# Performance work log

Hardware: AMD Instinct MI355X
Metric: run time of the kernel (lower is better)

The kernel has to match this reference:

```python
import jax, jax.numpy as jnp
import numpy as np
import math

EMBED_DIM = 512
NUM_HEADS = 8
NUM_EXPERTS = 16
TOP_K = 8
B, T = 2, 1024


def setup_inputs() -> dict:
    key = jax.random.key(0)
    ks = jax.random.split(key, 16)
    d, E = EMBED_DIM, NUM_EXPERTS
    hdim = 4 * d  # expert hidden width
    s = 0.02
    inp = {
        "x": jax.random.normal(ks[0], (B, T, d), jnp.float32),
        # RMSNorm params (init ones, matching torch module)
        "g": jnp.ones((d,), jnp.float32),
        "b": jnp.ones((d,), jnp.float32),
        # attention
        "c_attn_w": jax.random.normal(ks[1], (d, 3 * d), jnp.float32) * s,
        "c_attn_b": jnp.zeros((3 * d,), jnp.float32),
        "alpha": jnp.ones((NUM_HEADS,), jnp.float32),
        "c_proj_w": jax.random.normal(ks[2], (d, d), jnp.float32) * s,
        "c_proj_b": jnp.zeros((d,), jnp.float32),
        # router
        "router_w": jax.random.normal(ks[3], (d, E), jnp.float32) * s,
        "router_b": jnp.zeros((E,), jnp.float32),
        # stacked expert params: Linear(d,4d) -> SwiGLU(4d,4d) -> Linear(4d,d)
        "w_in": jax.random.normal(ks[4], (E, d, hdim), jnp.float32) * s,
        "b_in": jnp.zeros((E, hdim), jnp.float32),
        "w1": jax.random.normal(ks[5], (E, hdim, 2 * hdim), jnp.float32) * s,
        "b1": jnp.zeros((E, 2 * hdim), jnp.float32),
        "w2": jax.random.normal(ks[6], (E, hdim, hdim), jnp.float32) * s,
        "b2": jnp.zeros((E, hdim), jnp.float32),
        "w_out": jax.random.normal(ks[7], (E, hdim, d), jnp.float32) * s,
        "b_out": jnp.zeros((E, d), jnp.float32),
    }
    return inp


def _block(x, g, b, c_attn_w, c_attn_b, alpha, c_proj_w, c_proj_b,
           router_w, router_b, w_in, b_in, w1, b1, w2, b2, w_out, b_out):
    Bb, Tt, C = x.shape
    H = alpha.shape[0]
    hd = C // H
    E = router_b.shape[0]

    # RMSNorm (note: additive b, per original module)
    rms = jnp.sqrt(jnp.mean(x * x, axis=-1, keepdims=True) + 1e-6)
    xn = (x / rms) * g + b

    # QK-normalized causal attention
    qkv = xn @ c_attn_w + c_attn_b                      # [B,T,3C]
    q, k, v = jnp.split(qkv, 3, axis=-1)
    def heads(t):
        return t.reshape(Bb, Tt, H, hd).transpose(0, 2, 1, 3)  # [B,H,T,hd]
    q, k, v = heads(q), heads(k), heads(v)
    eps = 1e-5
    q_hat = q / (jnp.linalg.norm(q, axis=-1, keepdims=True) + eps)
    k_hat = k / (jnp.linalg.norm(k, axis=-1, keepdims=True) + eps)
    factor = (alpha * math.sqrt(hd)).reshape(1, H, 1, 1)
    q_scaled = q_hat * factor
    # SDPA default scale = 1/sqrt(head_dim)
    scores = jnp.einsum("bhqd,bhkd->bhqk", q_scaled, k_hat) / math.sqrt(hd)
    causal = jnp.tril(jnp.ones((Tt, Tt), bool))
    scores = jnp.where(causal, scores, -jnp.inf)
    att = jax.nn.softmax(scores, axis=-1)
    y = jnp.einsum("bhqk,bhkd->bhqd", att, v)
    y = y.transpose(0, 2, 1, 3).reshape(Bb, Tt, C)
    y = y @ c_proj_w + c_proj_b
    x = x + y

    # Router + top-8 normalized gates
    routes = jax.nn.softmax(x @ router_w + router_b, axis=-1)  # [B,T,E]
    probs, idx = jax.lax.top_k(routes, TOP_K)
    probs = probs / jnp.sum(probs, axis=-1, keepdims=True)
    # combine weights per expert: [B,T,E]
    gates = jnp.sum(jax.nn.one_hot(idx, E, dtype=x.dtype) * probs[..., None], axis=2)

    # Dense expert evaluation (faithful math: unselected tokens get zero gate)
    N = Bb * Tt
    xf = x.reshape(N, C)
    gf = gates.reshape(N, E)
    h = jnp.einsum("nd,edf->enf", xf, w_in) + b_in[:, None, :]      # [E,N,4d]
    c = jnp.einsum("enf,efg->eng", h, w1) + b1[:, None, :]          # [E,N,8d]
    a, bb2 = jnp.split(c, 2, axis=-1)
    s = (bb2 * jax.nn.sigmoid(bb2)) * a                              # SwiGLU
    o = jnp.einsum("enf,efg->eng", s, w2) + b2[:, None, :]          # [E,N,4d]
    eo = jnp.einsum("enf,efd->end", o, w_out) + b_out[:, None, :]   # [E,N,d]
    moe = jnp.einsum("end,ne->nd", eo, gf).reshape(Bb, Tt, C)
    return x + moe


def reference(x, g, b, c_attn_w, c_attn_b, alpha, c_proj_w, c_proj_b,
              router_w, router_b, w_in, b_in, w1, b1, w2, b2, w_out, b_out):
    return _block(x, g, b, c_attn_w, c_attn_b, alpha, c_proj_w, c_proj_b,
                  router_w, router_b, w_in, b_in, w1, b1, w2, b2, w_out, b_out)
```

## Files before the change

### kernel.cpp

```cpp
#include <hip/hip_runtime.h>
#include <stdint.h>

#define DEVI __device__ __forceinline__
#define FENCE() asm volatile("" ::: "memory")

typedef short short8 __attribute__((ext_vector_type(8)));
typedef short short4v __attribute__((ext_vector_type(4)));
typedef float f32x4 __attribute__((ext_vector_type(4)));

DEVI float bf2f(unsigned short s){ union{unsigned u; float f;} x; x.u = ((unsigned)s)<<16; return x.f; }
DEVI unsigned short f2bf(float f){ union{float f; unsigned u;} x; x.f=f; unsigned r = x.u + 0x7fff + ((x.u>>16)&1); return (unsigned short)(r>>16); }

DEVI void gload_lds16(const void* g, void* l){
  __builtin_amdgcn_global_load_lds((const __attribute__((address_space(1))) unsigned int*)g,
                                   (__attribute__((address_space(3))) unsigned int*)l, 16, 0, 0);
}

__global__ __launch_bounds__(256)
void transpose_cvt(const float* __restrict__ in, unsigned short* __restrict__ out, int K, int N)
{
  __shared__ float tile[32][33];
  size_t zoff = (size_t)blockIdx.z * K * N;
  const float* src = in + zoff;
  unsigned short* dst = out + zoff;
  int kb = blockIdx.y*32, nb = blockIdx.x*32;
  int t = threadIdx.x;
  int tr = t>>3, tc = (t&7)*4;
  float4 v = *(const float4*)(src + (size_t)(kb+tr)*N + nb + tc);
  tile[tr][tc+0]=v.x; tile[tr][tc+1]=v.y; tile[tr][tc+2]=v.z; tile[tr][tc+3]=v.w;
  __syncthreads();
  short4v ov;
  ov[0] = (short)f2bf(tile[tc+0][tr]);
  ov[1] = (short)f2bf(tile[tc+1][tr]);
  ov[2] = (short)f2bf(tile[tc+2][tr]);
  ov[3] = (short)f2bf(tile[tc+3][tr]);
  *(short4v*)(dst + (size_t)(nb+tr)*K + kb + tc) = ov;
}

__global__ __launch_bounds__(256)
void rmsnorm_k(const float* __restrict__ x, const float* __restrict__ gw,
               const float* __restrict__ bw, unsigned short* __restrict__ xn)
{
  int row = blockIdx.x*4 + (threadIdx.x>>6);
  int lane = threadIdx.x & 63;
  const float* xr = x + (size_t)row*512 + lane*8;
  float4 a = *(const float4*)xr;
  float4 c = *(const float4*)(xr+4);
  float ss = a.x*a.x+a.y*a.y+a.z*a.z+a.w*a.w + c.x*c.x+c.y*c.y+c.z*c.z+c.w*c.w;
  #pragma unroll
  for (int m=1;m<64;m<<=1) ss += __shfl_xor(ss, m);
  float inv = 1.0f / sqrtf(ss*(1.f/512.f) + 1e-6f);
  const float* gr = gw + lane*8; const float* br = bw + lane*8;
  float4 g0=*(const float4*)gr, g1=*(const float4*)(gr+4);
  float4 b0=*(const float4*)br, b1=*(const float4*)(br+4);
  short8 o;
  o[0]=(short)f2bf(a.x*inv*g0.x + b0.x);
  o[1]=(short)f2bf(a.y*inv*g0.y + b0.y);
  o[2]=(short)f2bf(a.z*inv*g0.z + b0.z);
  o[3]=(short)f2bf(a.w*inv*g0.w + b0.w);
  o[4]=(short)f2bf(c.x*inv*g1.x + b1.x);
  o[5]=(short)f2bf(c.y*inv*g1.y + b1.y);
  o[6]=(short)f2bf(c.z*inv*g1.z + b1.z);
  o[7]=(short)f2bf(c.w*inv*g1.w + b1.w);
  *(short8*)(xn + (size_t)row*512 + lane*8) = o;
}

template<int EPI>
__global__ __launch_bounds__(512, 2)
void gemm3(const unsigned short* __restrict__ A, const unsigned short* __restrict__ B,
           const float* __restrict__ bias,
           float* __restrict__ Cf, unsigned short* __restrict__ Ch,
           const unsigned short* __restrict__ aux,
           int M, int N, int K,
           const int* __restrict__ off, long long strideBz, long long strideBiasz)
{
  __shared__ char smem[147456];
  int z = blockIdx.z;
  int rowbase = 0, Mz = M;
  if (off){ rowbase = off[z]; Mz = off[z+1] - rowbase; }
  int row0 = blockIdx.y * 256;
  if (row0 >= Mz) return;
  int col0 = blockIdx.x * 128;
  const unsigned short* Ab = A + (size_t)(rowbase + row0) * K;
  const unsigned short* Bb = B + (size_t)z * strideBz + (size_t)col0 * K;
  const float* biasz = bias + (size_t)z * strideBiasz;

  int tid = threadIdx.x;
  int lane = tid & 63, w = tid >> 6;
  int lrow = lane & 15, lg = lane >> 4;
  int wr = w >> 1, wc = w & 1;

  f32x4 acc[4][4];
  #pragma unroll
  for (int i=0;i<4;i++){
    #pragma unroll
    for (int j=0;j<4;j++) acc[i][j] = f32x4{0.f,0.f,0.f,0.f};
  }

  int nkt = K >> 6;

  auto stage = [&](int kt2, int part){
    if (kt2 >= nkt) return;
    char* sA = smem + (kt2 % 3) * 49152;
    char* sB = sA + 32768;
    int k0 = kt2 << 6;
    #pragma unroll
    for (int i=0;i<2;i++){
      int s = (part*2 + i)*512 + tid;
      int r = s >> 3, kb = (s & 7) ^ (r & 7);
      gload_lds16(Ab + (size_t)r*K + k0 + kb*8, sA + s*16);
    }
    {
      int s = part*512 + tid;
      int r = s >> 3, kb = (s & 7) ^ (r & 7);
      gload_lds16(Bb + (size_t)r*K + k0 + kb*8, sB + s*16);
    }
  };

  stage(0,0); stage(0,1); stage(1,0); stage(1,1);
  asm volatile("s_waitcnt vmcnt(6)" ::: "memory");
  __builtin_amdgcn_s_barrier();
  FENCE();

  for (int kt = 0; kt < nkt; kt++){
    char* sA = smem + (kt % 3) * 49152;
    char* sB = sA + 32768;
    short8 bfr[4][2], afr[4][2];
    #pragma unroll
    for (int n=0;n<4;n++){
      int ct = wc*64 + n*16 + lrow;
      #pragma unroll
      for (int kk=0;kk<2;kk++){
        int kbb = lg + kk*4;
        bfr[n][kk] = *(const short8*)(sB + ct*128 + ((kbb ^ (ct&7))<<4));
      }
    }
    #pragma unroll
    for (int m=0;m<2;m++){
      int rt = wr*64 + m*16 + lrow;
      #pragma unroll
      for (int kk=0;kk<2;kk++){
        int kbb = lg + kk*4;
        afr[m][kk] = *(const short8*)(sA + rt*128 + ((kbb ^ (rt&7))<<4));
      }
    }
    stage(kt+2, 0);
    FENCE(); __builtin_amdgcn_s_barrier(); FENCE();
    __builtin_amdgcn_s_setprio(1);
    #pragma unroll
    for (int m=0;m<2;m++){
      #pragma unroll
      for (int n=0;n<4;n++){
        #pragma unroll
        for (int kk=0;kk<2;kk++)
          acc[m][n] = __builtin_amdgcn_mfma_f32_16x16x32_bf16(afr[m][kk], bfr[n][kk], acc[m][n], 0,0,0);
      }
    }
    __builtin_amdgcn_s_setprio(0);
    FENCE(); __builtin_amdgcn_s_barrier(); FENCE();
    #pragma unroll
    for (int m=2;m<4;m++){
      int rt = wr*64 + m*16 + lrow;
      #pragma unroll
      for (int kk=0;kk<2;kk++){
        int kbb = lg + kk*4;
        afr[m][kk] = *(const short8*)(sA + rt*128 + ((kbb ^ (rt&7))<<4));
      }
    }
    stage(kt+2, 1);
    FENCE(); __builtin_amdgcn_s_barrier(); FENCE();
    __builtin_amdgcn_s_setprio(1);
    #pragma unroll
    for (int m=2;m<4;m++){
      #pragma unroll
      for (int n=0;n<4;n++){
        #pragma unroll
        for (int kk=0;kk<2;kk++)
          acc[m][n] = __builtin_amdgcn_mfma_f32_16x16x32_bf16(afr[m][kk], bfr[n][kk], acc[m][n], 0,0,0);
      }
    }
    __builtin_amdgcn_s_setprio(0);
    asm volatile("s_waitcnt vmcnt(6)" ::: "memory");
    FENCE(); __builtin_amdgcn_s_barrier(); FENCE();
  }

  #pragma unroll
  for (int m=0;m<4;m++){
    int rloc = wr*64 + m*16 + lg*4;
    #pragma unroll
    for (int j=0;j<4;j++){
      int row = row0 + rloc + j;
      if (row < Mz){
        size_t rg = (size_t)(rowbase + row);
        #pragma unroll
        for (int n=0;n<4;n++){
          int col = col0 + wc*64 + n*16 + lrow;
          float v = acc[m][n][j] + biasz[col];
          size_t idx = rg * N + col;
          if constexpr (EPI == 0){
            Cf[idx] = v;
          } else if constexpr (EPI == 1){
            Ch[idx] = f2bf(v);
          } else {
            float a = bf2f(aux[idx]);
            float sg = v / (1.f + __expf(-v));
            Ch[idx] = f2bf(a * sg);
          }
        }
      }
    }
  }
}

__global__ __launch_bounds__(256)
void gemm_proj(const unsigned short* __restrict__ A, const unsigned short* __restrict__ B,
               const float* __restrict__ bias,
               float* __restrict__ Cf, unsigned short* __restrict__ Ch,
               const float* __restrict__ resid, int M, int N, int K)
{
  __shared__ char smem[32768];
  char* smA = smem; char* smB = smem + 16384;
  int row0 = blockIdx.y * 128;
  int col0 = blockIdx.x * 128;
  int t = threadIdx.x, w = t>>6, lane = t&63;
  int lrow = lane&15, lg = lane>>4;
  int wr = w>>1, wc = w&1;

  f32x4 acc[4][4];
  #pragma unroll
  for (int i=0;i<4;i++){
    #pragma unroll
    for (int j=0;j<4;j++) acc[i][j] = f32x4{0.f,0.f,0.f,0.f};
  }
  const size_t Abase = (size_t)row0 * K;
  const size_t Bbase = (size_t)col0 * K;
  int nkt = K >> 6;
  for (int kt=0; kt<nkt; kt++){
    __syncthreads();
    int k0 = kt*64;
    #pragma unroll
    for (int i=0;i<4;i++){
      int s = (i*4 + w)*64 + lane;
      int r = s>>3;
      int kb = (s&7) ^ (r&7);
      gload_lds16(A + Abase + (size_t)r*K + k0 + kb*8, smA + (size_t)(i*4+w)*1024);
      gload_lds16(B + Bbase + (size_t)r*K + k0 + kb*8, smB + (size_t)(i*4+w)*1024);
    }
    __syncthreads();
    #pragma unroll
    for (int ks=0; ks<2; ks++){
      short8 af[4], bf[4];
      int kbb = lg + ks*4;
      #pragma unroll
      for (int m=0;m<4;m++){
        int rt = wr*64 + m*16 + lrow;
        af[m] = *(const short8*)(smA + rt*128 + ((kbb ^ (rt&7))<<4));
      }
      #pragma unroll
      for (int n=0;n<4;n++){
        int rt = wc*64 + n*16 + lrow;
        bf[n] = *(const short8*)(smB + rt*128 + ((kbb ^ (rt&7))<<4));
      }
      #pragma unroll
      for (int m=0;m<4;m++){
        #pragma unroll
        for (int n=0;n<4;n++)
          acc[m][n] = __builtin_amdgcn_mfma_f32_16x16x32_bf16(af[m], bf[n], acc[m][n], 0,0,0);
      }
    }
  }
  #pragma unroll
  for (int m=0;m<4;m++){
    int rloc = wr*64 + m*16 + lg*4;
    #pragma unroll
    for (int j=0;j<4;j++){
      int row = row0 + rloc + j;
      size_t rg = (size_t)row;
      #pragma unroll
      for (int n=0;n<4;n++){
        int col = col0 + wc*64 + n*16 + lrow;
        float v = acc[m][n][j] + bias[col];
        size_t idx = rg * N + col;
        v += resid[idx];
        Cf[idx] = v;
        Ch[idx] = f2bf(v);
      }
    }
  }
}

__global__ __launch_bounds__(256)
void prep_qkv(const float* __restrict__ qkv, const float* __restrict__ alpha,
              unsigned short* __restrict__ q_s, unsigned short* __restrict__ k_hat,
              unsigned short* __restrict__ v_t)
{
  int idx = blockIdx.x*4 + (threadIdx.x>>6);
  int lane = threadIdx.x & 63;
  int h = idx & 7, bt = idx >> 3;
  size_t base = (size_t)bt*1536 + h*64 + lane;
  float qv = qkv[base], kv = qkv[base+512], vv = qkv[base+1024];
  float qs2 = qv*qv, ks2 = kv*kv;
  #pragma unroll
  for (int m=1;m<64;m<<=1){ qs2 += __shfl_xor(qs2, m); ks2 += __shfl_xor(ks2, m); }
  float qh = qv / (sqrtf(qs2) + 1e-5f) * alpha[h];
  float kh = kv / (sqrtf(ks2) + 1e-5f);
  int b = bt >> 10, tt = bt & 1023;
  size_t hb = ((size_t)(b*8+h))*1024*64;
  q_s[hb + (size_t)tt*64 + lane] = f2bf(qh);
  k_hat[hb + (size_t)tt*64 + lane] = f2bf(kh);
  v_t[((size_t)(b*8+h)*64 + lane)*1024 + tt] = f2bf(vv);
}

__global__ __launch_bounds__(256)
void attn_k(const unsigned short* __restrict__ q_s, const unsigned short* __restrict__ k_hat,
            const unsigned short* __restrict__ v_t, unsigned short* __restrict__ y)
{
  __shared__ char sm[51200];
  char* smK = sm + 18432;
  char* smV = sm + 34816;
  int qt = blockIdx.x, bh = blockIdx.y;
  int b = bh>>3, h = bh&7;
  int t = threadIdx.x, w = t>>6, lane = t&63;
  int lrow = lane&15, lg = lane>>4;
  int q0 = qt*128;
  const size_t hQK = (size_t)bh*1024*64;
  const size_t hV  = (size_t)bh*64*1024;

  #pragma unroll
  for (int i=0;i<4;i++){
    int s = (i*4+w)*64 + lane;
    int r = s>>3, kb = (s&7)^(r&7);
    gload_lds16(q_s + hQK + (size_t)(q0+r)*64 + kb*8, sm + (size_t)(i*4+w)*1024);
  }
  __syncthreads();
  short8 qf[2][2];
  #pragma unroll
  for (int mf=0;mf<2;mf++){
    #pragma unroll
    for (int ks=0;ks<2;ks++){
      int rt = w*32 + mf*16 + lrow;
      int kbb = lg + ks*4;
      qf[mf][ks] = *(const short8*)(sm + rt*128 + ((kbb^(rt&7))<<4));
    }
  }
  f32x4 oacc[2][4];
  #pragma unroll
  for (int i=0;i<2;i++){
    #pragma unroll
    for (int j=0;j<4;j++) oacc[i][j] = f32x4{0.f,0.f,0.f,0.f};
  }
  float mrun[2][4], lrun[2][4];
  #pragma unroll
  for (int i=0;i<2;i++){
    #pragma unroll
    for (int j=0;j<4;j++){ mrun[i][j] = -1e30f; lrun[i][j] = 0.f; }
  }
  char* Pw = sm + w*4608;

  for (int kt=0; kt<=qt; kt++){
    __syncthreads();
    int t0 = kt*128;
    #pragma unroll
    for (int i=0;i<4;i++){
      int s = (i*4+w)*64 + lane;
      int r = s>>3, kb = (s&7)^(r&7);
      gload_lds16(k_hat + hQK + (size_t)(t0+r)*64 + kb*8, smK + (size_t)(i*4+w)*1024);
    }
    #pragma unroll
    for (int i=0;i<4;i++){
      int s = (i*4+w)*64 + lane;
      int d = s>>4, kb2 = s&15;
      int kb = kb2 ^ (d&7);
      gload_lds16(v_t + hV + (size_t)d*1024 + t0 + kb*8, smV + (size_t)(i*4+w)*1024);
    }
    __syncthreads();

    f32x4 sacc[2][8];
    #pragma unroll
    for (int i=0;i<2;i++){
      #pragma unroll
      for (int j=0;j<8;j++) sacc[i][j] = f32x4{0.f,0.f,0.f,0.f};
    }
    #pragma unroll
    for (int ks=0;ks<2;ks++){
      short8 kf[8];
      int kbb = lg + ks*4;
      #pragma unroll
      for (int nf=0;nf<8;nf++){
        int rt = nf*16+lrow;
        kf[nf] = *(const short8*)(smK + rt*128 + ((kbb^(rt&7))<<4));
      }
      #pragma unroll
      for (int mf=0;mf<2;mf++){
        #pragma unroll
        for (int nf=0;nf<8;nf++)
          sacc[mf][nf] = __builtin_amdgcn_mfma_f32_16x16x32_bf16(qf[mf][ks], kf[nf], sacc[mf][nf], 0,0,0);
      }
    }
    if (kt == qt){
      #pragma unroll
      for (int mf=0;mf<2;mf++){
        #pragma unroll
        for (int nf=0;nf<8;nf++){
          #pragma unroll
          for (int j=0;j<4;j++){
            int qi = w*32+mf*16+lg*4+j;
            int ki = nf*16 + lrow;
            if (ki > qi) sacc[mf][nf][j] = -1e30f;
          }
        }
      }
    }
    #pragma unroll
    for (int mf=0;mf<2;mf++){
      #pragma unroll
      for (int j=0;j<4;j++){
        float mx = sacc[mf][0][j];
        #pragma unroll
        for (int nf=1;nf<8;nf++) mx = fmaxf(mx, sacc[mf][nf][j]);
        #pragma unroll
        for (int m=1;m<16;m<<=1) mx = fmaxf(mx, __shfl_xor(mx, m));
        float mnew = fmaxf(mrun[mf][j], mx);
        float sc = __expf(mrun[mf][j] - mnew);
        float rs = 0.f;
        #pragma unroll
        for (int nf=0;nf<8;nf++){
          float p = __expf(sacc[mf][nf][j] - mnew);
          sacc[mf][nf][j] = p; rs += p;
        }
        #pragma unroll
        for (int m=1;m<16;m<<=1) rs += __shfl_xor(rs, m);
        lrun[mf][j] = lrun[mf][j]*sc + rs;
        mrun[mf][j] = mnew;
        #pragma unroll
        for (int n2=0;n2<4;n2++) oacc[mf][n2][j] *= sc;
      }
    }
    #pragma unroll
    for (int half=0; half<2; half++){
      #pragma unroll
      for (int mf=0;mf<2;mf++){
        #pragma unroll
        for (int nfh=0;nfh<4;nfh++){
          int nf = half*4 + nfh;
          #pragma unroll
          for (int j=0;j<4;j++){
            int row = mf*16 + lg*4 + j;
            int col = nfh*16 + lrow;
            *(unsigned short*)(Pw + (row*72 + col)*2) = f2bf(sacc[mf][nf][j]);
          }
        }
      }
      #pragma unroll
      for (int k2=0;k2<2;k2++){
        int ks2 = half*2 + k2;
        short8 pf[2], vf[4];
        #pragma unroll
        for (int mf=0;mf<2;mf++)
          pf[mf] = *(const short8*)(Pw + (mf*16+lrow)*144 + lg*16 + k2*64);
        #pragma unroll
        for (int n2=0;n2<4;n2++){
          int d = n2*16+lrow;
          int kbb2 = lg + ks2*4;
          vf[n2] = *(const short8*)(smV + d*256 + ((kbb2^(d&7))<<4));
        }
        #pragma unroll
        for (int mf=0;mf<2;mf++){
          #pragma unroll
          for (int n2=0;n2<4;n2++)
            oacc[mf][n2] = __builtin_amdgcn_mfma_f32_16x16x32_bf16(pf[mf], vf[n2], oacc[mf][n2], 0,0,0);
        }
      }
    }
  }
  #pragma unroll
  for (int mf=0;mf<2;mf++){
    #pragma unroll
    for (int n2=0;n2<4;n2++){
      #pragma unroll
      for (int j=0;j<4;j++){
        float v = oacc[mf][n2][j] / lrun[mf][j];
        int qi = q0 + w*32 + mf*16 + lg*4 + j;
        int d = n2*16 + lrow;
        y[((size_t)(b*1024+qi))*512 + h*64 + d] = f2bf(v);
      }
    }
  }
}

__global__ __launch_bounds__(256)
void router_topk(const float* __restrict__ x2f, const float* __restrict__ rw,
                 const float* __restrict__ rb, float* __restrict__ gates)
{
  int tkn = blockIdx.x*4 + (threadIdx.x>>6);
  int lane = threadIdx.x & 63;
  int e = lane & 15, p = lane >> 4;
  const float* xr = x2f + (size_t)tkn*512;
  float part = 0.f;
  for (int d = p*128; d < p*128+128; d++)
    part += xr[d] * rw[d*16 + e];
  part += __shfl_xor(part, 16);
  part += __shfl_xor(part, 32);
  float logit = part + rb[e];
  float mx = logit;
  #pragma unroll
  for (int m=1;m<16;m<<=1) mx = fmaxf(mx, __shfl_xor(mx, m));
  float ex = __expf(logit - mx);
  float sm = ex;
  #pragma unroll
  for (int m=1;m<16;m<<=1) sm += __shfl_xor(sm, m);
  float prob = ex / sm;
  bool taken = false;
  float ssum = 0.f;
  #pragma unroll
  for (int r=0;r<8;r++){
    float cv = taken ? -1.f : prob;
    int ci = e;
    #pragma unroll
    for (int m=1;m<16;m<<=1){
      float ov = __shfl_xor(cv, m);
      int oi = __shfl_xor(ci, m);
      if (ov > cv || (ov == cv && oi < ci)){ cv = ov; ci = oi; }
    }
    if (e == ci) taken = true;
    ssum += cv;
  }
  if (lane < 16)
    gates[(size_t)tkn*16 + e] = taken ? prob / ssum : 0.f;
}

__global__ void listbuild(const float* __restrict__ gates, int* __restrict__ list,
                          int* __restrict__ slot, int* __restrict__ cnt)
{
  int e = blockIdx.x;
  int tid = threadIdx.x, w = tid>>6, lane = tid&63;
  __shared__ int sbase;
  __shared__ int wsum[4];
  if (tid==0) sbase = 0;
  __syncthreads();
  for (int c=0;c<8;c++){
    int tk = c*256 + tid;
    bool flag = gates[(size_t)tk*16 + e] > 0.f;
    unsigned long long bal = __ballot(flag);
    if (lane==0) wsum[w] = (int)__popcll(bal);
    __syncthreads();
    int wpref = 0;
    for (int i=0;i<w;i++) wpref += wsum[i];
    int tot = wsum[0]+wsum[1]+wsum[2]+wsum[3];
    int lpref = (int)__popcll(bal & ((1ull<<lane)-1ull));
    if (flag){
      int pos = sbase + wpref + lpref;
      list[e*2048 + pos] = tk;
      slot[(size_t)tk*16 + e] = pos;
    }
    __syncthreads();
    if (tid==0) sbase += tot;
    __syncthreads();
  }
  if (tid==0) cnt[e] = sbase;
}

__global__ void prefix_off(const int* __restrict__ cnt, int* __restrict__ off){
  if (threadIdx.x==0 && blockIdx.x==0){
    int a=0;
    for (int e=0;e<16;e++){ off[e]=a; a+=cnt[e]; }
    off[16]=a;
  }
}

__global__ __launch_bounds__(256)
void gather_rows(const unsigned short* __restrict__ x2h, const int* __restrict__ list,
                 const int* __restrict__ cnt, const int* __restrict__ off,
                 unsigned short* __restrict__ xe)
{
  int e = blockIdx.y;
  int s = blockIdx.x*4 + (threadIdx.x>>6);
  if (s >= cnt[e]) return;
  int lane = threadIdx.x & 63;
  int tk = list[e*2048 + s];
  *(short8*)(xe + ((size_t)(off[e]+s))*512 + lane*8) =
      *(const short8*)(x2h + (size_t)tk*512 + lane*8);
}

__global__ __launch_bounds__(256)
void combine_k(const float* __restrict__ x2f, const unsigned short* __restrict__ eo,
               const float* __restrict__ gates, const int* __restrict__ slot,
               const int* __restrict__ off, float* __restrict__ out)
{
  int tkn = blockIdx.x;
  __shared__ float gs[16];
  __shared__ int rws[16];
  int tid = threadIdx.x;
  if (tid < 16){
    float g = gates[(size_t)tkn*16 + tid];
    gs[tid] = g;
    rws[tid] = (g > 0.f) ? (off[tid] + slot[(size_t)tkn*16 + tid]) : 0;
  }
  __syncthreads();
  for (int d = tid; d < 512; d += 256){
    float v = x2f[(size_t)tkn*512 + d];
    #pragma unroll
    for (int e=0;e<16;e++){
      float g = gs[e];
      if (g > 0.f) v += g * bf2f(eo[(size_t)rws[e]*512 + d]);
    }
    out[(size_t)tkn*512 + d] = v;
  }
}

extern "C" void kernel_launch(void* const* d_in, const int* in_sizes, int n_in,
                              void* d_out, int out_size, void* d_ws, size_t ws_size,
                              hipStream_t stream) {
  (void)in_sizes; (void)n_in; (void)out_size; (void)ws_size;
  const float* x    = (const float*)d_in[0];
  const float* gw   = (const float*)d_in[1];
  const float* bw   = (const float*)d_in[2];
  const float* caw  = (const float*)d_in[3];
  const float* cab  = (const float*)d_in[4];
  const float* alpha= (const float*)d_in[5];
  const float* cpw  = (const float*)d_in[6];
  const float* cpb  = (const float*)d_in[7];
  const float* rw   = (const float*)d_in[8];
  const float* rb   = (const float*)d_in[9];
  const float* w_in = (const float*)d_in[10];
  const float* b_in = (const float*)d_in[11];
  const float* w1   = (const float*)d_in[12];
  const float* b1   = (const float*)d_in[13];
  const float* w2   = (const float*)d_in[14];
  const float* b2   = (const float*)d_in[15];
  const float* w_out= (const float*)d_in[16];
  const float* b_out= (const float*)d_in[17];

  char* ws = (char*)d_ws;
  size_t o = 0;
  auto alloc = [&](size_t bytes)->char*{
    char* p = ws + o;
    o += (bytes + 255) & ~(size_t)255;
    return p;
  };
  const size_t PADROWS = 16896;
  unsigned short* wT_attn = (unsigned short*)alloc(1536ull*512*2);
  unsigned short* wT_proj = (unsigned short*)alloc(512ull*512*2);
  unsigned short* wT_in   = (unsigned short*)alloc(16ull*2048*512*2);
  unsigned short* wT_1    = (unsigned short*)alloc(16ull*4096*2048*2);
  unsigned short* wT_2    = (unsigned short*)alloc(16ull*2048*2048*2);
  unsigned short* wT_out  = (unsigned short*)alloc(16ull*512*2048*2);
  unsigned short* xn      = (unsigned short*)alloc(2048ull*512*2);
  float*          qkv     = (float*)alloc(2048ull*1536*4);
  unsigned short* q_s     = (unsigned short*)alloc(2048ull*512*2);
  unsigned short* k_hat   = (unsigned short*)alloc(2048ull*512*2);
  unsigned short* v_t     = (unsigned short*)alloc(2048ull*512*2);
  unsigned short* ybuf    = (unsigned short*)alloc(2048ull*512*2);
  float*          x2f     = (float*)alloc(2048ull*512*4);
  unsigned short* x2h     = (unsigned short*)alloc(2048ull*512*2);
  float*          gates   = (float*)alloc(2048ull*16*4);
  int*            slot    = (int*)alloc(2048ull*16*4);
  int*            list    = (int*)alloc(16ull*2048*4);
  int*            cnt     = (int*)alloc(64);
  int*            off     = (int*)alloc(256);
  unsigned short* xe      = (unsigned short*)alloc(PADROWS*512*2);
  unsigned short* hbuf    = (unsigned short*)alloc(PADROWS*2048*2);
  unsigned short* c1buf   = (unsigned short*)alloc(PADROWS*2048*2);
  unsigned short* sbuf    = (unsigned short*)alloc(PADROWS*2048*2);
  unsigned short* eobuf   = xe;
  unsigned short* obuf    = hbuf;

  dim3 blk(256);
  dim3 blk5(512);
  transpose_cvt<<<dim3(1536/32, 512/32, 1), blk, 0, stream>>>(caw, wT_attn, 512, 1536);
  transpose_cvt<<<dim3(512/32, 512/32, 1), blk, 0, stream>>>(cpw, wT_proj, 512, 512);
  transpose_cvt<<<dim3(2048/32, 512/32, 16), blk, 0, stream>>>(w_in, wT_in, 512, 2048);
  transpose_cvt<<<dim3(4096/32, 2048/32, 16), blk, 0, stream>>>(w1, wT_1, 2048, 4096);
  transpose_cvt<<<dim3(2048/32, 2048/32, 16), blk, 0, stream>>>(w2, wT_2, 2048, 2048);
  transpose_cvt<<<dim3(512/32, 2048/32, 16), blk, 0, stream>>>(w_out, wT_out, 2048, 512);

  rmsnorm_k<<<512, blk, 0, stream>>>(x, gw, bw, xn);
  gemm3<0><<<dim3(12, 8, 1), blk5, 0, stream>>>(xn, wT_attn, cab, qkv, nullptr, nullptr,
                                                2048, 1536, 512, nullptr, 0, 0);
  prep_qkv<<<4096, blk, 0, stream>>>(qkv, alpha, q_s, k_hat, v_t);
  attn_k<<<dim3(8,16), blk, 0, stream>>>(q_s, k_hat, v_t, ybuf);
  gemm_proj<<<dim3(4,16,1), blk, 0, stream>>>(ybuf, wT_proj, cpb, x2f, x2h, x, 2048, 512, 512);
  router_topk<<<512, blk, 0, stream>>>(x2f, rw, rb, gates);
  listbuild<<<16, blk, 0, stream>>>(gates, list, slot, cnt);
  prefix_off<<<1, 64, 0, stream>>>(cnt, off);
  gather_rows<<<dim3(512,16), blk, 0, stream>>>(x2h, list, cnt, off, xe);

  gemm3<1><<<dim3(16,8,16), blk5, 0, stream>>>(xe, wT_in, b_in, nullptr, hbuf, nullptr,
                                               0, 2048, 512, off, 2048ll*512, 2048);
  gemm3<1><<<dim3(16,8,16), blk5, 0, stream>>>(hbuf, wT_1, b1, nullptr, c1buf, nullptr,
                                               0, 2048, 2048, off, 4096ll*2048, 4096);
  gemm3<2><<<dim3(16,8,16), blk5, 0, stream>>>(hbuf, wT_1 + 2048ull*2048, b1 + 2048, nullptr, sbuf,
                                               c1buf, 0, 2048, 2048, off, 4096ll*2048, 4096);
  gemm3<1><<<dim3(16,8,16), blk5, 0, stream>>>(sbuf, wT_2, b2, nullptr, obuf, nullptr,
                                               0, 2048, 2048, off, 2048ll*2048, 2048);
  gemm3<1><<<dim3(4,8,16), blk5, 0, stream>>>(obuf, wT_out, b_out, nullptr, eobuf, nullptr,
                                              0, 512, 2048, off, 512ll*2048, 512);
  combine_k<<<2048, blk, 0, stream>>>(x2f, eobuf, gates, slot, off, (float*)d_out);
}
```

Measured before the change: 1.173 ms.

## Enlarge GEMM tile to 256x256 with double-buffered LDS and quad MFMA phases

The bf16 MFMA GEMM output tile grows from 256x128 to 256x256, with the 8 waves arranged 2x4 so each wave computes 128x64. The LDS pipeline moves from three stages to two (128 KB), and global-to-LDS staging is split into four quarter loads spread across four MFMA phases. The aim is more operand reuse per byte loaded and fewer blocks for the expert and QKV GEMMs. In exchange, the per-thread accumulator and fragment state roughly doubles, which under the existing launch bounds risks register spills. Halving the block count also risks poorer occupancy and tail balance.

```diff
diff --git a/kernel.cpp b/kernel.cpp
--- a/kernel.cpp
+++ b/kernel.cpp
@@ -3,6 +3,7 @@
 
 #define DEVI __device__ __forceinline__
 #define FENCE() asm volatile("" ::: "memory")
+#define BAR() do{ FENCE(); __builtin_amdgcn_s_barrier(); FENCE(); }while(0)
 
 typedef short short8 __attribute__((ext_vector_type(8)));
 typedef short short4v __attribute__((ext_vector_type(4)));
@@ -65,22 +66,36 @@
   *(short8*)(xn + (size_t)row*512 + lane*8) = o;
 }
 
+#define MFMA_QUAD(MQ) do{ \
+  __builtin_amdgcn_s_setprio(1); \
+  _Pragma("unroll") \
+  for (int m=(MQ)*2; m<(MQ)*2+2; m++){ \
+    _Pragma("unroll") \
+    for (int n=0;n<4;n++){ \
+      _Pragma("unroll") \
+      for (int kk=0;kk<2;kk++) \
+        acc[m][n] = __builtin_amdgcn_mfma_f32_16x16x32_bf16(afr[m][kk], bfr[n][kk], acc[m][n], 0,0,0); \
+    } \
+  } \
+  __builtin_amdgcn_s_setprio(0); \
+}while(0)
+
 template<int EPI>
 __global__ __launch_bounds__(512, 2)
-void gemm3(const unsigned short* __restrict__ A, const unsigned short* __restrict__ B,
+void gemm8(const unsigned short* __restrict__ A, const unsigned short* __restrict__ B,
            const float* __restrict__ bias,
            float* __restrict__ Cf, unsigned short* __restrict__ Ch,
            const unsigned short* __restrict__ aux,
            int M, int N, int K,
            const int* __restrict__ off, long long strideBz, long long strideBiasz)
 {
-  __shared__ char smem[147456];
+  __shared__ char smem[131072];
   int z = blockIdx.z;
   int rowbase = 0, Mz = M;
   if (off){ rowbase = off[z]; Mz = off[z+1] - rowbase; }
   int row0 = blockIdx.y * 256;
   if (row0 >= Mz) return;
-  int col0 = blockIdx.x * 128;
+  int col0 = blockIdx.x * 256;
   const unsigned short* Ab = A + (size_t)(rowbase + row0) * K;
   const unsigned short* Bb = B + (size_t)z * strideBz + (size_t)col0 * K;
   const float* biasz = bias + (size_t)z * strideBiasz;
@@ -88,105 +103,79 @@
   int tid = threadIdx.x;
   int lane = tid & 63, w = tid >> 6;
   int lrow = lane & 15, lg = lane >> 4;
-  int wr = w >> 1, wc = w & 1;
-
-  f32x4 acc[4][4];
-  #pragma unroll
-  for (int i=0;i<4;i++){
+  int wm = w >> 2, wn = w & 3;
+
+  f32x4 acc[8][4];
+  #pragma unroll
+  for (int i=0;i<8;i++){
     #pragma unroll
     for (int j=0;j<4;j++) acc[i][j] = f32x4{0.f,0.f,0.f,0.f};
   }
 
   int nkt = K >> 6;
 
-  auto stage = [&](int kt2, int part){
+  auto stage = [&](int kt2, int H){
     if (kt2 >= nkt) return;
-    char* sA = smem + (kt2 % 3) * 49152;
-    char* sB = sA + 32768;
+    char* sl = smem + (size_t)(kt2 & 1) * 65536 + (size_t)H * 16384;
     int k0 = kt2 << 6;
+    const unsigned short* src = (H < 2) ? Ab : Bb;
+    int rbase = (H & 1) * 128;
     #pragma unroll
     for (int i=0;i<2;i++){
-      int s = (part*2 + i)*512 + tid;
-      int r = s >> 3, kb = (s & 7) ^ (r & 7);
-      gload_lds16(Ab + (size_t)r*K + k0 + kb*8, sA + s*16);
-    }
-    {
-      int s = part*512 + tid;
-      int r = s >> 3, kb = (s & 7) ^ (r & 7);
-      gload_lds16(Bb + (size_t)r*K + k0 + kb*8, sB + s*16);
+      int si = i*512 + tid;
+      int r = si >> 3, kb = (si & 7) ^ (r & 7);
+      gload_lds16(src + (size_t)(rbase + r)*K + k0 + kb*8, sl + si*16);
     }
   };
 
-  stage(0,0); stage(0,1); stage(1,0); stage(1,1);
+  stage(0,0); stage(0,1); stage(0,2); stage(0,3);
+  stage(1,0); stage(1,1); stage(1,2);
   asm volatile("s_waitcnt vmcnt(6)" ::: "memory");
-  __builtin_amdgcn_s_barrier();
-  FENCE();
+  BAR();
 
   for (int kt = 0; kt < nkt; kt++){
-    char* sA = smem + (kt % 3) * 49152;
-    char* sB = sA + 32768;
-    short8 bfr[4][2], afr[4][2];
+    char* sl = smem + (size_t)(kt & 1) * 65536;
+    char* sB = sl + 32768;
+    short8 afr[8][2], bfr[4][2];
     #pragma unroll
     for (int n=0;n<4;n++){
-      int ct = wc*64 + n*16 + lrow;
-      #pragma unroll
-      for (int kk=0;kk<2;kk++){
-        int kbb = lg + kk*4;
-        bfr[n][kk] = *(const short8*)(sB + ct*128 + ((kbb ^ (ct&7))<<4));
-      }
-    }
-    #pragma unroll
-    for (int m=0;m<2;m++){
-      int rt = wr*64 + m*16 + lrow;
-      #pragma unroll
-      for (int kk=0;kk<2;kk++){
-        int kbb = lg + kk*4;
-        afr[m][kk] = *(const short8*)(sA + rt*128 + ((kbb ^ (rt&7))<<4));
-      }
-    }
+      int ct = wn*64 + n*16 + lrow;
+      #pragma unroll
+      for (int kk=0;kk<2;kk++)
+        bfr[n][kk] = *(const short8*)(sB + ct*128 + (((lg + kk*4) ^ (ct&7))<<4));
+    }
+    #pragma unroll
+    for (int m=0;m<8;m++){
+      int rt = wm*128 + m*16 + lrow;
+      #pragma unroll
+      for (int kk=0;kk<2;kk++)
+        afr[m][kk] = *(const short8*)(sl + rt*128 + (((lg + kk*4) ^ (rt&7))<<4));
+    }
+    stage(kt+1, 3);
+    BAR();
+    asm volatile("s_waitcnt lgkmcnt(0)" ::: "memory");
+    __builtin_amdgcn_sched_barrier(0);
+    MFMA_QUAD(0);
+    BAR();
     stage(kt+2, 0);
-    FENCE(); __builtin_amdgcn_s_barrier(); FENCE();
-    __builtin_amdgcn_s_setprio(1);
-    #pragma unroll
-    for (int m=0;m<2;m++){
-      #pragma unroll
-      for (int n=0;n<4;n++){
-        #pragma unroll
-        for (int kk=0;kk<2;kk++)
-          acc[m][n] = __builtin_amdgcn_mfma_f32_16x16x32_bf16(afr[m][kk], bfr[n][kk], acc[m][n], 0,0,0);
-      }
-    }
-    __builtin_amdgcn_s_setprio(0);
-    FENCE(); __builtin_amdgcn_s_barrier(); FENCE();
-    #pragma unroll
-    for (int m=2;m<4;m++){
-      int rt = wr*64 + m*16 + lrow;
-      #pragma unroll
-      for (int kk=0;kk<2;kk++){
-        int kbb = lg + kk*4;
-        afr[m][kk] = *(const short8*)(sA + rt*128 + ((kbb ^ (rt&7))<<4));
-      }
-    }
+    BAR();
+    MFMA_QUAD(1);
+    BAR();
     stage(kt+2, 1);
-    FENCE(); __builtin_amdgcn_s_barrier(); FENCE();
-    __builtin_amdgcn_s_setprio(1);
-    #pragma unroll
-    for (int m=2;m<4;m++){
-      #pragma unroll
-      for (int n=0;n<4;n++){
-        #pragma unroll
-        for (int kk=0;kk<2;kk++)
-          acc[m][n] = __builtin_amdgcn_mfma_f32_16x16x32_bf16(afr[m][kk], bfr[n][kk], acc[m][n], 0,0,0);
-      }
-    }
-    __builtin_amdgcn_s_setprio(0);
-    asm volatile("s_waitcnt vmcnt(6)" ::: "memory");
-    FENCE(); __builtin_amdgcn_s_barrier(); FENCE();
-  }
-
-  #pragma unroll
-  for (int m=0;m<4;m++){
-    int rloc = wr*64 + m*16 + lg*4;
+    BAR();
+    MFMA_QUAD(2);
+    BAR();
+    stage(kt+2, 2);
+    if (kt + 2 < nkt) { asm volatile("s_waitcnt vmcnt(6)" ::: "memory"); }
+    else              { asm volatile("s_waitcnt vmcnt(0)" ::: "memory"); }
+    BAR();
+    MFMA_QUAD(3);
+    BAR();
+  }
+
+  #pragma unroll
+  for (int m=0;m<8;m++){
+    int rloc = wm*128 + m*16 + lg*4;
     #pragma unroll
     for (int j=0;j<4;j++){
       int row = row0 + rloc + j;
@@ -194,7 +183,7 @@
         size_t rg = (size_t)(rowbase + row);
         #pragma unroll
         for (int n=0;n<4;n++){
-          int col = col0 + wc*64 + n*16 + lrow;
+          int col = col0 + wn*64 + n*16 + lrow;
           float v = acc[m][n][j] + biasz[col];
           size_t idx = rg * N + col;
           if constexpr (EPI == 0){
@@ -675,8 +664,8 @@
   transpose_cvt<<<dim3(512/32, 2048/32, 16), blk, 0, stream>>>(w_out, wT_out, 2048, 512);
 
   rmsnorm_k<<<512, blk, 0, stream>>>(x, gw, bw, xn);
-  gemm3<0><<<dim3(12, 8, 1), blk5, 0, stream>>>(xn, wT_attn, cab, qkv, nullptr, nullptr,
-                                                2048, 1536, 512, nullptr, 0, 0);
+  gemm8<0><<<dim3(6, 8, 1), blk5, 0, stream>>>(xn, wT_attn, cab, qkv, nullptr, nullptr,
+                                               2048, 1536, 512, nullptr, 0, 0);
   prep_qkv<<<4096, blk, 0, stream>>>(qkv, alpha, q_s, k_hat, v_t);
   attn_k<<<dim3(8,16), blk, 0, stream>>>(q_s, k_hat, v_t, ybuf);
   gemm_proj<<<dim3(4,16,1), blk, 0, stream>>>(ybuf, wT_proj, cpb, x2f, x2h, x, 2048, 512, 512);
@@ -685,15 +674,15 @@
   prefix_off<<<1, 64, 0, stream>>>(cnt, off);
   gather_rows<<<dim3(512,16), blk, 0, stream>>>(x2h, list, cnt, off, xe);
 
-  gemm3<1><<<dim3(16,8,16), blk5, 0, stream>>>(xe, wT_in, b_in, nullptr, hbuf, nullptr,
-                                               0, 2048, 512, off, 2048ll*512, 2048);
-  gemm3<1><<<dim3(16,8,16), blk5, 0, stream>>>(hbuf, wT_1, b1, nullptr, c1buf, nullptr,
-                                               0, 2048, 2048, off, 4096ll*2048, 4096);
-  gemm3<2><<<dim3(16,8,16), blk5, 0, stream>>>(hbuf, wT_1 + 2048ull*2048, b1 + 2048, nullptr, sbuf,
-                                               c1buf, 0, 2048, 2048, off, 4096ll*2048, 4096);
-  gemm3<1><<<dim3(16,8,16), blk5, 0, stream>>>(sbuf, wT_2, b2, nullptr, obuf, nullptr,
-                                               0, 2048, 2048, off, 2048ll*2048, 2048);
-  gemm3<1><<<dim3(4,8,16), blk5, 0, stream>>>(obuf, wT_out, b_out, nullptr, eobuf, nullptr,
+  gemm8<1><<<dim3(8,8,16), blk5, 0, stream>>>(xe, wT_in, b_in, nullptr, hbuf, nullptr,
+                                              0, 2048, 512, off, 2048ll*512, 2048);
+  gemm8<1><<<dim3(8,8,16), blk5, 0, stream>>>(hbuf, wT_1, b1, nullptr, c1buf, nullptr,
+                                              0, 2048, 2048, off, 4096ll*2048, 4096);
+  gemm8<2><<<dim3(8,8,16), blk5, 0, stream>>>(hbuf, wT_1 + 2048ull*2048, b1 + 2048, nullptr, sbuf,
+                                              c1buf, 0, 2048, 2048, off, 4096ll*2048, 4096);
+  gemm8<1><<<dim3(8,8,16), blk5, 0, stream>>>(sbuf, wT_2, b2, nullptr, obuf, nullptr,
+                                              0, 2048, 2048, off, 2048ll*2048, 2048);
+  gemm8<1><<<dim3(2,8,16), blk5, 0, stream>>>(obuf, wT_out, b_out, nullptr, eobuf, nullptr,
                                               0, 512, 2048, off, 512ll*2048, 512);
   combine_k<<<2048, blk, 0, stream>>>(x2f, eobuf, gates, slot, off, (float*)d_out);
 }
```

Result: slower. 1.221 ms (+4.1%).
